# Kernel tuning notes

Hardware: AMD Instinct MI355X
Metric: run time of the kernel (lower is better)

The kernel has to match this reference:

```python
import jax, jax.numpy as jnp
import numpy as np

N, K, DIN, DOUT = 100000, 32, 128, 64
NEG = -9e15  # sentinel written into row 0 before the neighbor gather


def setup_inputs() -> dict:
    key = jax.random.key(0)
    k1, k2, k3, k4 = jax.random.split(key, 4)
    x = jax.random.normal(k1, (N, DIN), dtype=jnp.float32)
    a2a = jax.random.randint(k2, (N, K), 0, N, dtype=jnp.int64)
    W = jax.random.normal(k3, (DOUT, DIN), dtype=jnp.float32) * (1.0 / np.sqrt(DIN))
    b = jax.random.normal(k4, (DOUT,), dtype=jnp.float32) * 0.01
    return {"x": x, "a2a": a2a, "W": W, "b": b}


def reference(x, a2a, W, b):
    # h = Linear(x); row 0 overwritten with the -9e15 padding sentinel
    h = x @ W.T + b                                   # [N, DOUT]
    h = h.at[0].set(NEG)
    # attention logits: bmm(cat([h, h[a2a]], dim=1), h) without materializing the concat
    self_dot = jnp.sum(h * h, axis=-1, keepdims=True)  # [N, 1]
    nbr = h[a2a]                                       # [N, K, DOUT] gather
    nbr_dot = jnp.einsum('nkd,nd->nk', nbr, h)         # [N, K]
    logits = jnp.concatenate([self_dot, nbr_dot], axis=1)  # [N, K+1]
    att = jax.nn.softmax(logits, axis=1)
    out = h * att[:, 0:1]                              # scale by self-attention weight
    out = out.at[0].set(0.0)
    return out
```

## Files before the change

kernel.cpp:

```cpp
#include <hip/hip_runtime.h>

#define NN   100000
#define KK   32
#define DIN  128
#define DOUT 64
#define NEGV (-9e15f)

typedef __attribute__((ext_vector_type(8))) short bf16x8;
typedef __attribute__((ext_vector_type(4))) float f32x4;

__device__ __forceinline__ float bflo(unsigned u) { return __uint_as_float(u << 16); }
__device__ __forceinline__ float bfhi(unsigned u) { return __uint_as_float(u & 0xffff0000u); }
__device__ __forceinline__ ushort f2bf(float f) {
    unsigned u = __float_as_uint(f);
    return (ushort)((u + 0x7fffu + ((u >> 16) & 1u)) >> 16);
}
__device__ __forceinline__ unsigned pk2(float a, float b) {
    unsigned r;
    asm("v_cvt_pk_bf16_f32 %0, %1, %2" : "=v"(r) : "v"(a), "v"(b));
    return r;
}
__device__ __forceinline__ bf16x8 cvt8(float4 a, float4 b) {
    union { unsigned u[4]; bf16x8 v; } r;
    r.u[0] = pk2(a.x, a.y); r.u[1] = pk2(a.z, a.w);
    r.u[2] = pk2(b.x, b.y); r.u[3] = pk2(b.z, b.w);
    return r.v;
}

__global__ __launch_bounds__(256) void h_kernel(const float* __restrict__ x,
                                                const float* __restrict__ W,
                                                const float* __restrict__ b,
                                                ushort* __restrict__ hb) {
    const int t    = threadIdx.x;
    const int w    = t >> 6;
    const int lane = t & 63;
    const int lr   = lane & 15;
    const int lg   = lane >> 4;

    bf16x8 Bf[4][4];
    const float* wp = W + (size_t)lr * DIN + lg * 8;
#pragma unroll
    for (int ct = 0; ct < 4; ++ct)
#pragma unroll
        for (int ks = 0; ks < 4; ++ks) {
            const float* p = wp + ct * 16 * DIN + ks * 32;
            Bf[ct][ks] = cvt8(*(const float4*)p, *(const float4*)(p + 4));
        }

    float bias[4];
#pragma unroll
    for (int ct = 0; ct < 4; ++ct) bias[ct] = b[ct * 16 + lr];

    const int base = blockIdx.x * 128 + w * 16;
#pragma unroll
    for (int tile = 0; tile < 2; ++tile) {
        const int row0 = base + tile * 64;

        int ar = row0 + lr;
        if (ar > NN - 1) ar = NN - 1;
        const float* xp = x + (size_t)ar * DIN + lg * 8;

        bf16x8 Af[4];
#pragma unroll
        for (int ks = 0; ks < 4; ++ks)
            Af[ks] = cvt8(*(const float4*)(xp + ks * 32),
                          *(const float4*)(xp + ks * 32 + 4));

        f32x4 acc[4] = {{0.f,0.f,0.f,0.f},{0.f,0.f,0.f,0.f},
                        {0.f,0.f,0.f,0.f},{0.f,0.f,0.f,0.f}};
#pragma unroll
        for (int ct = 0; ct < 4; ++ct)
#pragma unroll
            for (int ks = 0; ks < 4; ++ks)
                acc[ct] = __builtin_amdgcn_mfma_f32_16x16x32_bf16(
                    Af[ks], Bf[ct][ks], acc[ct], 0, 0, 0);

#pragma unroll
        for (int ct = 0; ct < 4; ++ct)
#pragma unroll
            for (int j = 0; j < 4; ++j) {
                const int m = row0 + lg * 4 + j;
                if (m < NN) {
                    const float v = (m == 0) ? NEGV : (acc[ct][j] + bias[ct]);
                    hb[(size_t)m * DOUT + ct * 16 + lr] = f2bf(v);
                }
            }
    }
}

__global__ __launch_bounds__(256) void att_kernel(const ushort* __restrict__ hb,
                                                  const int* __restrict__ a2a,
                                                  float* __restrict__ out) {
    const int t    = threadIdx.x;
    const int wid  = t >> 6;
    const int lane = t & 63;
    const int n    = blockIdx.x * 4 + wid;

    const ushort* hbn = hb + (size_t)n * DOUT;
    const float hv = bflo((unsigned)hbn[lane]);

    float sp = hv * hv;
#pragma unroll
    for (int q = 1; q <= 32; q <<= 1) sp += __shfl_xor(sp, q);

    const int k    = lane >> 1;
    const int half = lane & 1;
    const int idx  = a2a[n * KK + k];

    const uint4* nb = reinterpret_cast<const uint4*>(hb + (size_t)idx * DOUT) + half * 4;
    const uint4* un = reinterpret_cast<const uint4*>(hbn) + half * 4;

    float d = 0.f;
#pragma unroll
    for (int i = 0; i < 4; ++i) {
        const uint4 v = nb[i];
        const uint4 u = un[i];
        d = fmaf(bflo(v.x), bflo(u.x), d); d = fmaf(bfhi(v.x), bfhi(u.x), d);
        d = fmaf(bflo(v.y), bflo(u.y), d); d = fmaf(bfhi(v.y), bfhi(u.y), d);
        d = fmaf(bflo(v.z), bflo(u.z), d); d = fmaf(bfhi(v.z), bfhi(u.z), d);
        d = fmaf(bflo(v.w), bflo(u.w), d); d = fmaf(bfhi(v.w), bfhi(u.w), d);
    }
    d += __shfl_xor(d, 1);

    float m = d;
#pragma unroll
    for (int q = 2; q <= 32; q <<= 1) m = fmaxf(m, __shfl_xor(m, q));
    m = fmaxf(m, sp);

    float e = __expf(d - m);
    float s = e;
#pragma unroll
    for (int q = 1; q <= 32; q <<= 1) s += __shfl_xor(s, q);
    s *= 0.5f;

    const float es = __expf(sp - m);
    const float w0 = es / (es + s);

    float o = hv * w0;
    if (n == 0) o = 0.f;
    out[(size_t)n * DOUT + lane] = o;
}

extern "C" void kernel_launch(void* const* d_in, const int* in_sizes, int n_in,
                              void* d_out, int out_size, void* d_ws, size_t ws_size,
                              hipStream_t stream) {
    const float* x   = (const float*)d_in[0];
    const int*   a2a = (const int*)d_in[1];
    const float* W   = (const float*)d_in[2];
    const float* b   = (const float*)d_in[3];
    float*       out = (float*)d_out;
    ushort*      hb  = (ushort*)d_ws;

    h_kernel<<<(NN + 127) / 128, 256, 0, stream>>>(x, W, b, hb);
    att_kernel<<<NN / 4, 256, 0, stream>>>(hb, a2a, out);
}
```

Baseline: 162.6 us.

## Compute neighbor dot products with MFMA and process two nodes per wave

Replaces the per-lane scalar FMA dot products between each node and its 32 gathered neighbors with bf16 MFMA instructions, treating the neighbor rows as the A matrix and the node row as B. Each wave now handles two nodes in an unrolled loop, and the grid shrinks to match. The softmax max and sum reductions use fewer cross-lane shuffles because each lane holds several logits. The kernel is likely bound by memory on the random gathers, so the saving in ALU and shuffle work may matter little. Only one column of each MFMA output is used, so most of the matrix-unit work is redundant.

```diff
diff --git a/kernel.cpp b/kernel.cpp
--- a/kernel.cpp
+++ b/kernel.cpp
@@ -94,51 +94,70 @@
     const int t    = threadIdx.x;
     const int wid  = t >> 6;
     const int lane = t & 63;
-    const int n    = blockIdx.x * 4 + wid;
+    const int lr   = lane & 15;
+    const int lg   = lane >> 4;
+    const int n0   = blockIdx.x * 8 + wid * 2;
 
-    const ushort* hbn = hb + (size_t)n * DOUT;
-    const float hv = bflo((unsigned)hbn[lane]);
+#pragma unroll
+    for (int r = 0; r < 2; ++r) {
+        const int n = n0 + r;
+        const ushort* hbn = hb + (size_t)n * DOUT;
 
-    float sp = hv * hv;
+        const bf16x8 B0 = *(const bf16x8*)(hbn + lg * 8);
+        const bf16x8 B1 = *(const bf16x8*)(hbn + 32 + lg * 8);
+
+        const int i0 = a2a[n * KK + lr];
+        const int i1 = a2a[n * KK + 16 + lr];
+        const ushort* p0 = hb + (size_t)i0 * DOUT + lg * 8;
+        const ushort* p1 = hb + (size_t)i1 * DOUT + lg * 8;
+
+        const bf16x8 A00 = *(const bf16x8*)p0;
+        const bf16x8 A01 = *(const bf16x8*)(p0 + 32);
+        const bf16x8 A10 = *(const bf16x8*)p1;
+        const bf16x8 A11 = *(const bf16x8*)(p1 + 32);
+
+        const float hv = bflo((unsigned)hbn[lane]);
+
+        f32x4 d0 = {0.f, 0.f, 0.f, 0.f};
+        f32x4 d1 = {0.f, 0.f, 0.f, 0.f};
+        d0 = __builtin_amdgcn_mfma_f32_16x16x32_bf16(A00, B0, d0, 0, 0, 0);
+        d0 = __builtin_amdgcn_mfma_f32_16x16x32_bf16(A01, B1, d0, 0, 0, 0);
+        d1 = __builtin_amdgcn_mfma_f32_16x16x32_bf16(A10, B0, d1, 0, 0, 0);
+        d1 = __builtin_amdgcn_mfma_f32_16x16x32_bf16(A11, B1, d1, 0, 0, 0);
+
+        union { bf16x8 v; unsigned u[4]; } ub0, ub1;
+        ub0.v = B0; ub1.v = B1;
+        float sp = 0.f;
 #pragma unroll
-    for (int q = 1; q <= 32; q <<= 1) sp += __shfl_xor(sp, q);
+        for (int i = 0; i < 4; ++i) {
+            float a = bflo(ub0.u[i]), c = bfhi(ub0.u[i]);
+            float e = bflo(ub1.u[i]), g = bfhi(ub1.u[i]);
+            sp = fmaf(a, a, sp); sp = fmaf(c, c, sp);
+            sp = fmaf(e, e, sp); sp = fmaf(g, g, sp);
+        }
+        sp += __shfl_xor(sp, 16);
+        sp += __shfl_xor(sp, 32);
 
-    const int k    = lane >> 1;
-    const int half = lane & 1;
-    const int idx  = a2a[n * KK + k];
+        float m = fmaxf(fmaxf(fmaxf(d0[0], d0[1]), fmaxf(d0[2], d0[3])),
+                        fmaxf(fmaxf(d1[0], d1[1]), fmaxf(d1[2], d1[3])));
+        m = fmaxf(m, __shfl_xor(m, 16));
+        m = fmaxf(m, __shfl_xor(m, 32));
+        m = fmaxf(m, sp);
 
-    const uint4* nb = reinterpret_cast<const uint4*>(hb + (size_t)idx * DOUT) + half * 4;
-    const uint4* un = reinterpret_cast<const uint4*>(hbn) + half * 4;
+        float s = __expf(d0[0] - m) + __expf(d0[1] - m) +
+                  __expf(d0[2] - m) + __expf(d0[3] - m) +
+                  __expf(d1[0] - m) + __expf(d1[1] - m) +
+                  __expf(d1[2] - m) + __expf(d1[3] - m);
+        s += __shfl_xor(s, 16);
+        s += __shfl_xor(s, 32);
 
-    float d = 0.f;
-#pragma unroll
-    for (int i = 0; i < 4; ++i) {
-        const uint4 v = nb[i];
-        const uint4 u = un[i];
-        d = fmaf(bflo(v.x), bflo(u.x), d); d = fmaf(bfhi(v.x), bfhi(u.x), d);
-        d = fmaf(bflo(v.y), bflo(u.y), d); d = fmaf(bfhi(v.y), bfhi(u.y), d);
-        d = fmaf(bflo(v.z), bflo(u.z), d); d = fmaf(bfhi(v.z), bfhi(u.z), d);
-        d = fmaf(bflo(v.w), bflo(u.w), d); d = fmaf(bfhi(v.w), bfhi(u.w), d);
+        const float es = __expf(sp - m);
+        const float w0 = es / (es + s);
+
+        float o = hv * w0;
+        if (n == 0) o = 0.f;
+        out[(size_t)n * DOUT + lane] = o;
     }
-    d += __shfl_xor(d, 1);
-
-    float m = d;
-#pragma unroll
-    for (int q = 2; q <= 32; q <<= 1) m = fmaxf(m, __shfl_xor(m, q));
-    m = fmaxf(m, sp);
-
-    float e = __expf(d - m);
-    float s = e;
-#pragma unroll
-    for (int q = 1; q <= 32; q <<= 1) s += __shfl_xor(s, q);
-    s *= 0.5f;
-
-    const float es = __expf(sp - m);
-    const float w0 = es / (es + s);
-
-    float o = hv * w0;
-    if (n == 0) o = 0.f;
-    out[(size_t)n * DOUT + lane] = o;
 }
 
 extern "C" void kernel_launch(void* const* d_in, const int* in_sizes, int n_in,
@@ -152,5 +171,5 @@
     ushort*      hb  = (ushort*)d_ws;
 
     h_kernel<<<(NN + 127) / 128, 256, 0, stream>>>(x, W, b, hb);
-    att_kernel<<<NN / 4, 256, 0, stream>>>(hb, a2a, out);
+    att_kernel<<<NN / 8, 256, 0, stream>>>(hb, a2a, out);
 }
```

Measured after the change: 169.8 us. 4.4% more time.
